# Optimization experiments

Measured on AMD Instinct MI355X. Metric: run time of the kernel, lower is better.

The kernel has to match this reference:

```python
import jax, jax.numpy as jnp
import numpy as np

N, E, H = 4096, 32768, 4
NUM_GRAPHS = 8
NEG_SLOPE_ATT = 0.2   # GATConv internal leaky_relu
NEG_SLOPE_ACT = 0.01  # F.leaky_relu default


def _glorot(k, shape):
    lim = (6.0 / (shape[0] + shape[-1])) ** 0.5
    return jax.random.uniform(k, shape, jnp.float32, -lim, lim)


def setup_inputs() -> dict:
    key = jax.random.key(0)
    ks = jax.random.split(key, 24)
    d = {}
    d["x_graph"] = jax.random.normal(ks[0], (N, 256), jnp.float32)
    d["action"] = jax.random.normal(ks[1], (N, 128), jnp.float32)
    d["temp_img"] = jax.random.normal(ks[2], (N, 128), jnp.float32)
    d["edge_attr"] = jax.random.normal(ks[3], (E, 16), jnp.float32)
    d["edge_index"] = jax.random.randint(ks[4], (2, E), 0, N)
    d["batch"] = jnp.sort(jax.random.randint(ks[5], (N,), 0, NUM_GRAPHS))
    # conv1: GATConv(512 -> 512, heads=4, edge_dim=16)
    d["W1"] = _glorot(ks[6], (512, H * 512))
    d["att_src1"] = _glorot(ks[7], (H, 512))
    d["att_dst1"] = _glorot(ks[8], (H, 512))
    d["att_edge1"] = _glorot(ks[9], (H, 512))
    d["We1"] = _glorot(ks[10], (16, H * 512))
    d["b1"] = jnp.zeros((H * 512,), jnp.float32)
    # conv2: GATConv(2048 -> 2048, heads=4, edge_dim=16)
    d["W2"] = _glorot(ks[11], (2048, H * 2048))
    d["att_src2"] = _glorot(ks[12], (H, 2048))
    d["att_dst2"] = _glorot(ks[13], (H, 2048))
    d["att_edge2"] = _glorot(ks[14], (H, 2048))
    d["We2"] = _glorot(ks[15], (16, H * 2048))
    d["b2"] = jnp.zeros((H * 2048,), jnp.float32)
    # fc_output: Linear(512*heads*heads=8192 -> 256)
    d["Wout"] = _glorot(ks[16], (8192, 256))
    d["bout"] = jnp.zeros((256,), jnp.float32)
    return d


def _gat(x, src, dst, eattr, W, a_s, a_d, a_e, We, b, C):
    # PyG GATConv: shared lin for src/dst, edge features in attention, softmax per dst.
    h = (x @ W).reshape(N, H, C)             # [N,H,C]
    ea = (eattr @ We).reshape(-1, H, C)      # [Ef,H,C]
    e = (h * a_s).sum(-1)[src] + (h * a_d).sum(-1)[dst] + (ea * a_e).sum(-1)  # [Ef,H]
    e = jax.nn.leaky_relu(e, NEG_SLOPE_ATT)
    m = jax.ops.segment_max(e, dst, num_segments=N)      # self-loops ensure every dst occupied
    ex = jnp.exp(e - m[dst])
    s = jax.ops.segment_sum(ex, dst, num_segments=N)
    alpha = ex / s[dst]                                   # [Ef,H]
    out = jax.ops.segment_sum(alpha[:, :, None] * h[src], dst, num_segments=N)  # [N,H,C]
    return out.reshape(N, H * C) + b


def _forward(x_graph, action, temp_img, edge_attr,
             W1, att_src1, att_dst1, att_edge1, We1, b1,
             W2, att_src2, att_dst2, att_edge2, We2, b2,
             Wout, bout, edge_index, batch):
    x = jnp.concatenate([x_graph, action, temp_img], axis=1)  # [N,512]
    src, dst = edge_index[0], edge_index[1]
    # add self-loops with fill_value='mean' for edge_attr (mean of incoming edge attrs)
    deg = jax.ops.segment_sum(jnp.ones((E,), x.dtype), dst, num_segments=N)
    loop_attr = jax.ops.segment_sum(edge_attr, dst, num_segments=N) / jnp.maximum(deg, 1.0)[:, None]
    loop = jnp.arange(N)
    src_f = jnp.concatenate([src, loop])
    dst_f = jnp.concatenate([dst, loop])
    ea_f = jnp.concatenate([edge_attr, loop_attr], axis=0)
    x = jax.nn.leaky_relu(_gat(x, src_f, dst_f, ea_f, W1, att_src1, att_dst1, att_edge1, We1, b1, 512), NEG_SLOPE_ACT)
    x = jax.nn.leaky_relu(_gat(x, src_f, dst_f, ea_f, W2, att_src2, att_dst2, att_edge2, We2, b2, 2048), NEG_SLOPE_ACT)
    x = jax.nn.leaky_relu(x @ Wout + bout, NEG_SLOPE_ACT)     # [N,256]
    sums = jax.ops.segment_sum(x, batch, num_segments=NUM_GRAPHS)
    cnt = jax.ops.segment_sum(jnp.ones((N,), x.dtype), batch, num_segments=NUM_GRAPHS)
    return sums / jnp.maximum(cnt, 1.0)[:, None]              # [NUM_GRAPHS,256]


def reference(x_graph, action, temp_img, edge_attr,
              W1, att_src1, att_dst1, att_edge1, We1, b1,
              W2, att_src2, att_dst2, att_edge2, We2, b2,
              Wout, bout, edge_index, batch):
    return _forward(x_graph, action, temp_img, edge_attr,
                    W1, att_src1, att_dst1, att_edge1, We1, b1,
                    W2, att_src2, att_dst2, att_edge2, We2, b2,
                    Wout, bout, edge_index, batch)
```

## Files before the change

### kernel.cpp

```cpp
#include <hip/hip_runtime.h>
#include <math.h>

constexpr int Nn  = 4096;
constexpr int Ne  = 32768;
constexpr int NEf = Ne + Nn;

constexpr size_t OFF_X    = 0;
constexpr size_t OFF_WT1H = 0;
constexpr size_t OFF_WT1L = 524288;
constexpr size_t OFF_Z1HI = 2097152;
constexpr size_t OFF_Z1LO = 6291456;
constexpr size_t OFF_X3   = 2097152;
constexpr size_t OFF_PART = 2097152;
constexpr size_t OFF_X2HI = 10485760;
constexpr size_t OFF_X2LO = 14680064;
constexpr size_t OFF_H    = 18874368;
constexpr size_t OFF_WOH  = 25165824;
constexpr size_t OFF_WOL  = 26214400;
constexpr size_t OFF_YP   = 27262976;
constexpr size_t OFF_LP  = 31457280;
constexpr size_t OFF_WS1 = OFF_LP  + 65536;
constexpr size_t OFF_WD1 = OFF_WS1 + 2048;
constexpr size_t OFF_WS2 = OFF_WD1 + 2048;
constexpr size_t OFF_WD2 = OFF_WS2 + 8192;
constexpr size_t OFF_AE1 = OFF_WD2 + 8192;
constexpr size_t OFF_AE2 = OFF_AE1 + 64;
constexpr size_t OFF_AS1 = OFF_AE2 + 64;
constexpr size_t OFF_AD1 = OFF_AS1 + 16384;
constexpr size_t OFF_AS2 = OFF_AD1 + 16384;
constexpr size_t OFF_AD2 = OFF_AS2 + 16384;
constexpr size_t OFF_EB  = OFF_AD2 + 16384;
constexpr size_t OFF_AL  = OFF_EB  + (size_t)NEf*4;
constexpr size_t OFF_I   = OFF_AL  + (size_t)NEf*4;
constexpr size_t I_DEG = 0;
constexpr size_t I_RP  = 4096;
constexpr size_t I_CUR = 8200;
constexpr size_t I_EID = 12296;
constexpr size_t WS_FLOATS = OFF_I + I_EID + (size_t)NEf + 64;

using bf16x8 = __bf16 __attribute__((ext_vector_type(8)));
using f16x8  = _Float16 __attribute__((ext_vector_type(8)));
using f32x4  = float __attribute__((ext_vector_type(4)));

__device__ __forceinline__ float wred64(float v){
#pragma unroll
  for (int o = 32; o > 0; o >>= 1) v += __shfl_down(v, o, 64);
  return v;
}
__device__ __forceinline__ float lrelu(float v, float s){ return v > 0.f ? v : s * v; }

__device__ __forceinline__ unsigned short f2bf(float x){
  unsigned int u = __float_as_uint(x);
  unsigned int r = (u + 0x7FFFu + ((u >> 16) & 1u)) >> 16;
  return (unsigned short)r;
}
__device__ __forceinline__ float bf2f(unsigned short h){
  return __uint_as_float((unsigned int)h << 16);
}
__device__ __forceinline__ void split2(float x, unsigned short& h, unsigned short& l){
  h = f2bf(x);
  l = f2bf(x - bf2f(h));
}
__device__ __forceinline__ unsigned short f2h(float x){
  _Float16 h = (_Float16)x;
  return __builtin_bit_cast(unsigned short, h);
}
__device__ __forceinline__ float h2f(unsigned short u){
  return (float)__builtin_bit_cast(_Float16, u);
}
__device__ __forceinline__ void split2h(float x, unsigned short& h, unsigned short& l){
  _Float16 hh = (_Float16)x;
  h = __builtin_bit_cast(unsigned short, hh);
  _Float16 ll = (_Float16)(x - (float)hh);
  l = __builtin_bit_cast(unsigned short, ll);
}
__device__ __forceinline__ void gload16(const void* g, void* l){
  __builtin_amdgcn_global_load_lds((const __attribute__((address_space(1))) void*)g,
                                   (__attribute__((address_space(3))) void*)l, 16, 0, 0);
}

__global__ void k_concat(const float* __restrict__ xg, const float* __restrict__ ac,
                         const float* __restrict__ ti, float* __restrict__ x){
  int i = blockIdx.x * 256 + threadIdx.x;
  int n = i >> 9, c = i & 511;
  float v;
  if (c < 256)      v = xg[(size_t)n*256 + c];
  else if (c < 384) v = ac[(size_t)n*128 + (c-256)];
  else              v = ti[(size_t)n*128 + (c-384)];
  x[i] = v;
}

__global__ void k_count(const int* __restrict__ ei, int* __restrict__ deg){
  int e = blockIdx.x * 256 + threadIdx.x;
  if (e < Ne) atomicAdd(&deg[ei[Ne + e]], 1);
}

__global__ void k_scan(const int* __restrict__ deg, int* __restrict__ rowptr, int* __restrict__ cursor){
  __shared__ int sd[1024];
  int t = threadIdx.x;
  int v[4]; int s = 0;
#pragma unroll
  for (int i = 0; i < 4; i++){ v[i] = s; s += deg[t*4 + i] + 1; }
  sd[t] = s;
  __syncthreads();
  for (int off = 1; off < 1024; off <<= 1){
    int x = (t >= off) ? sd[t - off] : 0;
    __syncthreads();
    sd[t] += x;
    __syncthreads();
  }
  int base = (t == 0) ? 0 : sd[t - 1];
#pragma unroll
  for (int i = 0; i < 4; i++){ int rp = base + v[i]; rowptr[t*4 + i] = rp; cursor[t*4 + i] = rp; }
  if (t == 1023) rowptr[4096] = sd[1023];
}

__global__ void k_fill(const int* __restrict__ ei, int* __restrict__ cursor, int* __restrict__ eids){
  int e = blockIdx.x * 256 + threadIdx.x;
  if (e >= NEf) return;
  int d = (e < Ne) ? ei[Ne + e] : (e - Ne);
  int p = atomicAdd(&cursor[d], 1);
  eids[p] = e;
}

__global__ void k_sort(const int* __restrict__ rowptr, int* __restrict__ eids){
  int n = blockIdx.x * 64 + threadIdx.x;
  if (n >= Nn) return;
  int b = rowptr[n], e = rowptr[n + 1];
  for (int i = b + 1; i < e; i++){
    int key = eids[i]; int j = i - 1;
    while (j >= b && eids[j] > key){ eids[j+1] = eids[j]; j--; }
    eids[j+1] = key;
  }
}

__global__ void k_loopattr(const float* __restrict__ eattr, const int* __restrict__ rowptr,
                           const int* __restrict__ eids, float* __restrict__ lp){
  int idx = blockIdx.x * 256 + threadIdx.x;
  int n = idx >> 4, a = idx & 15;
  if (n >= Nn) return;
  int b = rowptr[n], e = rowptr[n + 1];
  float s = 0.f; int cnt = 0;
  for (int j = b; j < e; ++j){
    int id = eids[j];
    if (id < Ne){ s += eattr[(size_t)id*16 + a]; cnt++; }
  }
  lp[(size_t)n*16 + a] = s / fmaxf((float)cnt, 1.f);
}

__global__ void k_proj(const float* __restrict__ W, const float* __restrict__ a_s,
                       const float* __restrict__ a_d, float* __restrict__ Ws,
                       float* __restrict__ Wd, int K, int C){
  int gid = blockIdx.x * 256 + threadIdx.x;
  int wave = gid >> 6, lane = gid & 63;
  int h = wave & 3, k = wave >> 2;
  if (k >= K) return;
  const float* wrow = W + (size_t)k * (4*C) + (size_t)h * C;
  const float* ar = a_s + (size_t)h * C;
  const float* dr = a_d + (size_t)h * C;
  float ps = 0.f, pd = 0.f;
  for (int c = lane; c < C; c += 64){ float w = wrow[c]; ps += w * ar[c]; pd += w * dr[c]; }
  ps = wred64(ps); pd = wred64(pd);
  if (lane == 0){ Ws[k*4 + h] = ps; Wd[k*4 + h] = pd; }
}

__global__ void k_aeproj(const float* __restrict__ We, const float* __restrict__ ae,
                         float* __restrict__ outp, int C){
  int gid = blockIdx.x * 256 + threadIdx.x;
  int wave = gid >> 6, lane = gid & 63;
  int h = wave & 3, k = wave >> 2;
  if (k >= 16) return;
  const float* wrow = We + (size_t)k * (4*C) + (size_t)h * C;
  const float* ar = ae + (size_t)h * C;
  float s = 0.f;
  for (int c = lane; c < C; c += 64) s += wrow[c] * ar[c];
  s = wred64(s);
  if (lane == 0) outp[k*4 + h] = s;
}

template<bool HALF>
__global__ __launch_bounds__(256) void k_asad(const void* __restrict__ xp, const void* __restrict__ xlp,
                      const float* __restrict__ Ws,
                      const float* __restrict__ Wd, float* __restrict__ as_,
                      float* __restrict__ ad_, int D){
  int n = blockIdx.x, t = threadIdx.x;
  float p[8] = {0,0,0,0,0,0,0,0};
  if (HALF){
    const unsigned short* rh = (const unsigned short*)xp + (size_t)n * D;
    const unsigned short* rl = (const unsigned short*)xlp + (size_t)n * D;
    for (int c = t; c < D; c += 256){
      float xv = h2f(rh[c]) + h2f(rl[c]);
      float4 ws4 = *(const float4*)&Ws[c*4];
      float4 wd4 = *(const float4*)&Wd[c*4];
      p[0] += xv * ws4.x; p[1] += xv * ws4.y; p[2] += xv * ws4.z; p[3] += xv * ws4.w;
      p[4] += xv * wd4.x; p[5] += xv * wd4.y; p[6] += xv * wd4.z; p[7] += xv * wd4.w;
    }
  } else {
    const float* row = (const float*)xp + (size_t)n * D;
    for (int c = t; c < D; c += 256){
      float xv = row[c];
      float4 ws4 = *(const float4*)&Ws[c*4];
      float4 wd4 = *(const float4*)&Wd[c*4];
      p[0] += xv * ws4.x; p[1] += xv * ws4.y; p[2] += xv * ws4.z; p[3] += xv * ws4.w;
      p[4] += xv * wd4.x; p[5] += xv * wd4.y; p[6] += xv * wd4.z; p[7] += xv * wd4.w;
    }
  }
  __shared__ float sm[4][8];
  int lane = t & 63, wid = t >> 6;
#pragma unroll
  for (int q = 0; q < 8; q++){
    float v = wred64(p[q]);
    if (lane == 0) sm[wid][q] = v;
  }
  __syncthreads();
  if (t < 8){
    float s = sm[0][t] + sm[1][t] + sm[2][t] + sm[3][t];
    if (t < 4) as_[(size_t)n*4 + t] = s;
    else       ad_[(size_t)n*4 + (t-4)] = s;
  }
}

__global__ void k_edge(const float* __restrict__ eattr, const float* __restrict__ lp,
                       const int* __restrict__ ei, const float* __restrict__ as_,
                       const float* __restrict__ ad_, const float* __restrict__ aep,
                       float* __restrict__ ebuf){
  int e = blockIdx.x * 256 + threadIdx.x;
  if (e >= NEf) return;
  int s, d; const float* ea;
  if (e < Ne){ s = ei[e]; d = ei[Ne + e]; ea = eattr + (size_t)e * 16; }
  else { s = e - Ne; d = e - Ne; ea = lp + (size_t)(e - Ne) * 16; }
  float eav[16];
#pragma unroll
  for (int k = 0; k < 16; k++) eav[k] = ea[k];
#pragma unroll
  for (int h = 0; h < 4; h++){
    float v = as_[(size_t)s*4 + h] + ad_[(size_t)d*4 + h];
#pragma unroll
    for (int k = 0; k < 16; k++) v += eav[k] * aep[k*4 + h];
    ebuf[(size_t)e*4 + h] = lrelu(v, 0.2f);
  }
}

__global__ __launch_bounds__(256) void k_softmax(const int* __restrict__ rowptr, const int* __restrict__ eids,
                          const float* __restrict__ ebuf, float* __restrict__ alpha){
  const int wid = threadIdx.x >> 6, lane = threadIdx.x & 63;
  const int n = blockIdx.x * 4 + wid;
  const int b = rowptr[n], e = rowptr[n + 1];
  float4 m = {-1e30f, -1e30f, -1e30f, -1e30f};
  for (int j = b + lane; j < e; j += 64){
    float4 ev = *(const float4*)&ebuf[(size_t)eids[j]*4];
    m.x = fmaxf(m.x, ev.x); m.y = fmaxf(m.y, ev.y);
    m.z = fmaxf(m.z, ev.z); m.w = fmaxf(m.w, ev.w);
  }
#pragma unroll
  for (int o = 32; o > 0; o >>= 1){
    m.x = fmaxf(m.x, __shfl_xor(m.x, o, 64));
    m.y = fmaxf(m.y, __shfl_xor(m.y, o, 64));
    m.z = fmaxf(m.z, __shfl_xor(m.z, o, 64));
    m.w = fmaxf(m.w, __shfl_xor(m.w, o, 64));
  }
  float4 s = {0.f, 0.f, 0.f, 0.f};
  for (int j = b + lane; j < e; j += 64){
    int eid = eids[j];
    float4 ev = *(const float4*)&ebuf[(size_t)eid*4];
    float4 ex = { expf(ev.x - m.x), expf(ev.y - m.y), expf(ev.z - m.z), expf(ev.w - m.w) };
    *(float4*)&alpha[(size_t)eid*4] = ex;
    s.x += ex.x; s.y += ex.y; s.z += ex.z; s.w += ex.w;
  }
#pragma unroll
  for (int o = 32; o > 0; o >>= 1){
    s.x += __shfl_xor(s.x, o, 64);
    s.y += __shfl_xor(s.y, o, 64);
    s.z += __shfl_xor(s.z, o, 64);
    s.w += __shfl_xor(s.w, o, 64);
  }
  float4 r = { 1.f/s.x, 1.f/s.y, 1.f/s.z, 1.f/s.w };
  for (int j = b + lane; j < e; j += 64){
    int eid = eids[j];
    float4 av = *(const float4*)&alpha[(size_t)eid*4];
    av.x *= r.x; av.y *= r.y; av.z *= r.z; av.w *= r.w;
    *(float4*)&alpha[(size_t)eid*4] = av;
  }
}

__global__ __launch_bounds__(256) void k_agg1_split(const float* __restrict__ x, const float* __restrict__ alpha,
                      const int* __restrict__ rowptr, const int* __restrict__ eids,
                      const int* __restrict__ ei, unsigned short* __restrict__ z1hi,
                      unsigned short* __restrict__ z1lo){
  int n = blockIdx.x, t = threadIdx.x;
  float2 a0 = {0,0}, a1 = {0,0}, a2 = {0,0}, a3 = {0,0};
  int b = rowptr[n], e = rowptr[n + 1];
  for (int j = b; j < e; ++j){
    int eid = eids[j];
    int s = (eid < Ne) ? ei[eid] : (eid - Ne);
    float4 av = *(const float4*)&alpha[(size_t)eid*4];
    float2 xv = *(const float2*)&x[(size_t)s*512 + t*2];
    a0.x += av.x*xv.x; a0.y += av.x*xv.y;
    a1.x += av.y*xv.x; a1.y += av.y*xv.y;
    a2.x += av.z*xv.x; a2.y += av.z*xv.y;
    a3.x += av.w*xv.x; a3.y += av.w*xv.y;
  }
  size_t base = (size_t)n*2048 + t*2;
  float2 av[4] = {a0, a1, a2, a3};
#pragma unroll
  for (int h = 0; h < 4; h++){
    ushort2 hh, ll;
    split2(av[h].x, hh.x, ll.x);
    split2(av[h].y, hh.y, ll.y);
    *(ushort2*)&z1hi[base + h*512] = hh;
    *(ushort2*)&z1lo[base + h*512] = ll;
  }
}

__global__ __launch_bounds__(256) void k_agg2b(const unsigned short* __restrict__ H,
                      const float* __restrict__ alpha,
                      const int* __restrict__ rowptr, const int* __restrict__ eids,
                      const int* __restrict__ ei, unsigned short* __restrict__ x3,
                      const float* __restrict__ b2, int h){
  int n = blockIdx.x, t = threadIdx.x;
  float acc[8] = {0,0,0,0,0,0,0,0};
  int b = rowptr[n], e = rowptr[n + 1];
  for (int j = b; j < e; ++j){
    int eid = eids[j];
    int s = (eid < Ne) ? ei[eid] : (eid - Ne);
    float a = alpha[(size_t)eid*4 + h];
    f16x8 hv = *(const f16x8*)&H[(size_t)s*2048 + t*8];
#pragma unroll
    for (int q = 0; q < 8; q++) acc[q] += a * (float)hv[q];
  }
  const float* bb = b2 + (size_t)h*2048 + t*8;
  ushort4 o0, o1;
  float4 b0 = *(const float4*)bb;
  float4 b1 = *(const float4*)(bb + 4);
  o0.x = f2h(lrelu(acc[0] + b0.x, 0.01f)); o0.y = f2h(lrelu(acc[1] + b0.y, 0.01f));
  o0.z = f2h(lrelu(acc[2] + b0.z, 0.01f)); o0.w = f2h(lrelu(acc[3] + b0.w, 0.01f));
  o1.x = f2h(lrelu(acc[4] + b1.x, 0.01f)); o1.y = f2h(lrelu(acc[5] + b1.y, 0.01f));
  o1.z = f2h(lrelu(acc[6] + b1.z, 0.01f)); o1.w = f2h(lrelu(acc[7] + b1.w, 0.01f));
  size_t base = (size_t)n*2048 + t*8;
  *(ushort4*)&x3[base]     = o0;
  *(ushort4*)&x3[base + 4] = o1;
}

template<bool HALF, bool STORELO>
__global__ __launch_bounds__(256) void k_wsplit(const float* __restrict__ W, int ldw, int coloff, int K,
                       unsigned short* __restrict__ whi, unsigned short* __restrict__ wlo){
  __shared__ float tile[32][33];
  int bk = blockIdx.x * 32, bn = blockIdx.y * 32;
  int tx = threadIdx.x & 31, ty = threadIdx.x >> 5;
#pragma unroll
  for (int i = 0; i < 4; i++){
    int k = bk + ty + i*8;
    tile[ty + i*8][tx] = W[(size_t)k*ldw + coloff + bn + tx];
  }
  __syncthreads();
#pragma unroll
  for (int i = 0; i < 4; i++){
    int n = bn + ty + i*8;
    float v = tile[tx][ty + i*8];
    unsigned short hh, ll;
    if (HALF) split2h(v, hh, ll); else split2(v, hh, ll);
    whi[(size_t)n*K + bk + tx] = hh;
    if (STORELO) wlo[(size_t)n*K + bk + tx] = ll;
  }
}

__global__ __launch_bounds__(512) void k_gemm256(
    const unsigned short* __restrict__ Ah, const unsigned short* __restrict__ Al,
    const unsigned short* __restrict__ Bh, unsigned short* __restrict__ Cout)
{
  __shared__ __align__(16) unsigned short lds[49152];
  const int t = threadIdx.x;
  const int bid = blockIdx.y * 8 + blockIdx.x;
  const int sbid = (bid & 7) * 32 + (bid >> 3);
  const int brow = (sbid >> 3) * 128, bcol = (sbid & 7) * 256;
  const int w = t >> 6, lane = t & 63;
  const int wm = (w >> 2) * 64, wn = (w & 3) * 64;
  constexpr int BUF = 16384, BOFF = 8192;

  const int asr = t >> 3;
  const int ascc = (t & 7) ^ (asr & 7);
  const unsigned short* asrc = (ascc < 4 ? Ah : Al) + (size_t)(brow + asr)*2048 + (size_t)(ascc & 3)*8;
  const int bsr = t >> 2;
  const int bscc = (t & 3) ^ ((bsr >> 1) & 3);
  const unsigned short* bsrc = Bh + (size_t)(bcol + bsr)*2048 + (size_t)bscc*8;
  const int adst = w * 512;
  const int bdst = BOFF + w * 512;

  const int fr = lane & 15, kc = lane >> 4;
  const int aswz = (kc ^ (lane & 7)) * 8;
  const int bswz = (kc ^ ((lane >> 1) & 3)) * 8;
  int aoff[4], boff[4];
#pragma unroll
  for (int m = 0; m < 4; m++) aoff[m] = (wm + m*16 + fr)*64 + aswz;
#pragma unroll
  for (int n = 0; n < 4; n++) boff[n] = BOFF + (wn + n*16 + fr)*32 + bswz;

  f32x4 acc[4][4];
#pragma unroll
  for (int m = 0; m < 4; m++)
#pragma unroll
    for (int n = 0; n < 4; n++) acc[m][n] = f32x4{0.f, 0.f, 0.f, 0.f};

  gload16(asrc,                        &lds[adst]);
  gload16(asrc + (size_t)64*2048,      &lds[4096 + adst]);
  gload16(bsrc,                        &lds[bdst]);
  gload16(bsrc + (size_t)128*2048,     &lds[4096 + bdst]);
  gload16(asrc + 32,                   &lds[BUF + adst]);
  gload16(asrc + (size_t)64*2048 + 32, &lds[BUF + 4096 + adst]);
  gload16(bsrc + 32,                   &lds[BUF + bdst]);
  gload16(bsrc + (size_t)128*2048 + 32,&lds[BUF + 4096 + bdst]);
  asm volatile("s_waitcnt vmcnt(4)" ::: "memory");
  __builtin_amdgcn_s_barrier();
  __builtin_amdgcn_sched_barrier(0);

  for (int kt = 0; kt < 64; ++kt){
    const int bufo = (kt % 3) * BUF;
    const int nbo  = ((kt + 2) % 3) * BUF;
    const size_t nko = (size_t)(kt + 2) * 32;
    const bool pf = (kt + 2) < 64;

    if (pf){
      gload16(asrc + nko,                    &lds[nbo + adst]);
      gload16(asrc + (size_t)64*2048 + nko,  &lds[nbo + 4096 + adst]);
      gload16(bsrc + nko,                    &lds[nbo + bdst]);
      gload16(bsrc + (size_t)128*2048 + nko, &lds[nbo + 4096 + bdst]);
    }

    f16x8 ah[4], al[4], bfr[4];
#pragma unroll
    for (int m = 0; m < 4; m++){
      ah[m] = *(const f16x8*)&lds[bufo + aoff[m]];
      al[m] = *(const f16x8*)&lds[bufo + (aoff[m] ^ 32)];
    }
#pragma unroll
    for (int n = 0; n < 4; n++) bfr[n] = *(const f16x8*)&lds[bufo + boff[n]];

    __builtin_amdgcn_s_setprio(1);
#pragma unroll
    for (int n = 0; n < 4; n++){
#pragma unroll
      for (int m = 0; m < 4; m++) acc[m][n] = __builtin_amdgcn_mfma_f32_16x16x32_f16(ah[m], bfr[n], acc[m][n], 0, 0, 0);
#pragma unroll
      for (int m = 0; m < 4; m++) acc[m][n] = __builtin_amdgcn_mfma_f32_16x16x32_f16(al[m], bfr[n], acc[m][n], 0, 0, 0);
    }
    __builtin_amdgcn_s_setprio(0);

    if (pf) asm volatile("s_waitcnt vmcnt(4)" ::: "memory");
    else    asm volatile("s_waitcnt vmcnt(0)" ::: "memory");
    __builtin_amdgcn_s_barrier();
    __builtin_amdgcn_sched_barrier(0);
  }

#pragma unroll
  for (int m = 0; m < 4; m++){
    const int row0 = brow + wm + m*16 + kc*4;
#pragma unroll
    for (int n = 0; n < 4; n++){
      const int col = bcol + wn + n*16 + fr;
#pragma unroll
      for (int r = 0; r < 4; r++)
        Cout[(size_t)(row0 + r)*2048 + col] = f2h(acc[m][n][r]);
    }
  }
}

template<int KLEN, bool EXACTA, bool HALF, int OUTMODE, bool BETA1, bool ACT, bool HASBIAS>
__global__ __launch_bounds__(256) void k_gemm2(
    const unsigned short* __restrict__ Ah, const unsigned short* __restrict__ Al, int lda, size_t az,
    const unsigned short* __restrict__ Bh, const unsigned short* __restrict__ Bl, int ldb, size_t bz,
    void* __restrict__ Cout, void* __restrict__ Cout2, int ldc, size_t cz,
    const float* __restrict__ bias, size_t biasz)
{
  __shared__ unsigned short lds[16384];
  const int t = threadIdx.x;
  const int z = blockIdx.z;
  const int brow = blockIdx.y * 128, bcol = blockIdx.x * 128;
  const int wid = t >> 6, lane = t & 63;
  const int wm = (wid >> 1) * 64, wn = (wid & 1) * 64;

  const int sr = t >> 3, sc = t & 7;
  const int scc = sc ^ (sr & 7);
  const unsigned short* asrc = (scc < 4 ? Ah : Al) + (size_t)(brow + sr)*lda + (size_t)z*az + (size_t)(scc & 3)*8;
  const unsigned short* bsrc = (scc < 4 ? Bh : Bl) + (size_t)(bcol + sr)*ldb + (size_t)z*bz + (size_t)(scc & 3)*8;
  unsigned short* adst = &lds[(size_t)wid * 512];
  unsigned short* bdst = &lds[8192 + (size_t)wid * 512];

  const int fr = lane & 15, kc = lane >> 4;
  const int swz = ((kc ^ (lane & 7)) << 3);
  int aoff[4], boff[4];
#pragma unroll
  for (int m = 0; m < 4; m++) aoff[m] = (wm + m*16 + fr)*64 + swz;
#pragma unroll
  for (int n = 0; n < 4; n++) boff[n] = 8192 + (wn + n*16 + fr)*64 + swz;

  f32x4 acc[4][4];
#pragma unroll
  for (int m = 0; m < 4; m++)
#pragma unroll
    for (int n = 0; n < 4; n++) acc[m][n] = f32x4{0.f, 0.f, 0.f, 0.f};

  for (int kt = 0; kt < KLEN/32; ++kt){
    const size_t ko = (size_t)kt * 32;
#pragma unroll
    for (int i = 0; i < 4; i++){
      gload16(asrc + (size_t)i*32*lda + ko, adst + i*2048);
      gload16(bsrc + (size_t)i*32*ldb + ko, bdst + i*2048);
    }
    __syncthreads();

    if (HALF){
      f16x8 ah[4], bh[4], bl[4];
#pragma unroll
      for (int m = 0; m < 4; m++) ah[m] = *(const f16x8*)&lds[aoff[m]];
#pragma unroll
      for (int n = 0; n < 4; n++){
        bh[n] = *(const f16x8*)&lds[boff[n]];
        bl[n] = *(const f16x8*)&lds[boff[n] ^ 32];
      }
#pragma unroll
      for (int m = 0; m < 4; m++)
#pragma unroll
        for (int n = 0; n < 4; n++){
          acc[m][n] = __builtin_amdgcn_mfma_f32_16x16x32_f16(ah[m], bh[n], acc[m][n], 0, 0, 0);
          acc[m][n] = __builtin_amdgcn_mfma_f32_16x16x32_f16(ah[m], bl[n], acc[m][n], 0, 0, 0);
        }
    } else {
      bf16x8 ah[4], al[4], bh[4], bl[4];
#pragma unroll
      for (int m = 0; m < 4; m++){
        ah[m] = *(const bf16x8*)&lds[aoff[m]];
        if (!EXACTA) al[m] = *(const bf16x8*)&lds[aoff[m] ^ 32];
      }
#pragma unroll
      for (int n = 0; n < 4; n++){
        bh[n] = *(const bf16x8*)&lds[boff[n]];
        bl[n] = *(const bf16x8*)&lds[boff[n] ^ 32];
      }
#pragma unroll
      for (int m = 0; m < 4; m++)
#pragma unroll
        for (int n = 0; n < 4; n++){
          acc[m][n] = __builtin_amdgcn_mfma_f32_16x16x32_bf16(ah[m], bh[n], acc[m][n], 0, 0, 0);
          acc[m][n] = __builtin_amdgcn_mfma_f32_16x16x32_bf16(ah[m], bl[n], acc[m][n], 0, 0, 0);
          if (!EXACTA)
            acc[m][n] = __builtin_amdgcn_mfma_f32_16x16x32_bf16(al[m], bh[n], acc[m][n], 0, 0, 0);
        }
    }
    __syncthreads();
  }

  float bv[4] = {0.f, 0.f, 0.f, 0.f};
  if (HASBIAS){
#pragma unroll
    for (int n = 0; n < 4; n++) bv[n] = bias[(size_t)z*biasz + bcol + wn + n*16 + fr];
  }
  float* Cf = (float*)Cout + (size_t)z*cz;
  unsigned short* Cb = (unsigned short*)Cout + (size_t)z*cz;
  unsigned short* Cl = (unsigned short*)Cout2 + (size_t)z*cz;
#pragma unroll
  for (int m = 0; m < 4; m++){
    const int row0 = brow + wm + m*16 + kc*4;
#pragma unroll
    for (int n = 0; n < 4; n++){
      const int col = bcol + wn + n*16 + fr;
#pragma unroll
      for (int r = 0; r < 4; r++){
        float v = acc[m][n][r] + bv[n];
        if (ACT) v = lrelu(v, 0.01f);
        size_t idx = (size_t)(row0 + r)*ldc + col;
        if (OUTMODE == 0){
          float* cp = &Cf[idx];
          if (BETA1) v += *cp;
          *cp = v;
        } else if (OUTMODE == 1){
          Cb[idx] = f2bf(v);
        } else {
          unsigned short hh, ll; split2h(v, hh, ll);
          Cb[idx] = hh; Cl[idx] = ll;
        }
      }
    }
  }
}

__global__ void k_gsum(const float* __restrict__ yp, const float* __restrict__ bout,
                       const int* __restrict__ batch, float* __restrict__ part){
  const int s = blockIdx.x, g = blockIdx.y, t = threadIdx.x;
  __shared__ int sb[2];
  if (t < 2){
    int key = g + t, lo = 0, hi = Nn;
    while (lo < hi){ int mid = (lo + hi) >> 1; if (batch[mid] < key) lo = mid + 1; else hi = mid; }
    sb[t] = lo;
  }
  __syncthreads();
  const int b = sb[0], e = sb[1];
  const size_t P = (size_t)Nn * 256;
  float acc = 0.f;
  float bt = bout[t];
  for (int n = b + s; n < e; n += 32){
    size_t i = (size_t)n*256 + t;
    float v = yp[i] + yp[P + i] + yp[2*P + i] + yp[3*P + i] + bt;
    acc += lrelu(v, 0.01f);
  }
  part[(size_t)(g*32 + s)*256 + t] = acc;
}

__global__ void k_gfin(const float* __restrict__ part, const int* __restrict__ batch,
                       float* __restrict__ out){
  const int g = blockIdx.x, t = threadIdx.x;
  __shared__ int sb[2];
  if (t < 2){
    int key = g + t, lo = 0, hi = Nn;
    while (lo < hi){ int mid = (lo + hi) >> 1; if (batch[mid] < key) lo = mid + 1; else hi = mid; }
    sb[t] = lo;
  }
  __syncthreads();
  const int cnt = sb[1] - sb[0];
  float s = 0.f;
#pragma unroll
  for (int k = 0; k < 32; k++) s += part[(size_t)(g*32 + k)*256 + t];
  out[g*256 + t] = s / fmaxf((float)cnt, 1.f);
}

extern "C" void kernel_launch(void* const* d_in, const int* in_sizes, int n_in,
                              void* d_out, int out_size, void* d_ws, size_t ws_size,
                              hipStream_t stream){
  const float* xg    = (const float*)d_in[0];
  const float* ac    = (const float*)d_in[1];
  const float* ti    = (const float*)d_in[2];
  const float* eattr = (const float*)d_in[3];
  const int*   ei    = (const int*)  d_in[4];
  const int*   batch = (const int*)  d_in[5];
  const float* W1    = (const float*)d_in[6];
  const float* as1w  = (const float*)d_in[7];
  const float* ad1w  = (const float*)d_in[8];
  const float* ae1w  = (const float*)d_in[9];
  const float* We1   = (const float*)d_in[10];
  const float* b1    = (const float*)d_in[11];
  const float* W2    = (const float*)d_in[12];
  const float* as2w  = (const float*)d_in[13];
  const float* ad2w  = (const float*)d_in[14];
  const float* ae2w  = (const float*)d_in[15];
  const float* We2   = (const float*)d_in[16];
  const float* b2    = (const float*)d_in[17];
  const float* Wout  = (const float*)d_in[18];
  const float* bout  = (const float*)d_in[19];
  float* out = (float*)d_out;
  float* ws  = (float*)d_ws;
  if (ws_size < WS_FLOATS * sizeof(float)) return;
  int* iws = (int*)(ws + OFF_I);

  unsigned short* z1hi = (unsigned short*)(ws + OFF_Z1HI);
  unsigned short* z1lo = (unsigned short*)(ws + OFF_Z1LO);
  unsigned short* wt1h = (unsigned short*)(ws + OFF_WT1H);
  unsigned short* wt1l = (unsigned short*)(ws + OFF_WT1L);
  unsigned short* x2hi = (unsigned short*)(ws + OFF_X2HI);
  unsigned short* x2lo = (unsigned short*)(ws + OFF_X2LO);
  unsigned short* whi  = (unsigned short*)(ws + OFF_X);
  unsigned short* woh  = (unsigned short*)(ws + OFF_WOH);
  unsigned short* wol  = (unsigned short*)(ws + OFF_WOL);
  unsigned short* Hb   = (unsigned short*)(ws + OFF_H);
  unsigned short* x3   = (unsigned short*)(ws + OFF_X3);

  hipMemsetAsync(iws + I_DEG, 0, Nn * sizeof(int), stream);
  k_concat <<<8192, 256, 0, stream>>>(xg, ac, ti, ws + OFF_X);
  k_count  <<<128,  256, 0, stream>>>(ei, iws + I_DEG);
  k_scan   <<<1,   1024, 0, stream>>>(iws + I_DEG, iws + I_RP, iws + I_CUR);
  k_fill   <<<144,  256, 0, stream>>>(ei, iws + I_CUR, iws + I_EID);
  k_sort   <<<64,    64, 0, stream>>>(iws + I_RP, iws + I_EID);
  k_loopattr<<<256, 256, 0, stream>>>(eattr, iws + I_RP, iws + I_EID, ws + OFF_LP);

  k_proj   <<<512,  256, 0, stream>>>(W1, as1w, ad1w, ws + OFF_WS1, ws + OFF_WD1, 512, 512);
  k_proj   <<<2048, 256, 0, stream>>>(W2, as2w, ad2w, ws + OFF_WS2, ws + OFF_WD2, 2048, 2048);
  k_aeproj <<<16,   256, 0, stream>>>(We1, ae1w, ws + OFF_AE1, 512);
  k_aeproj <<<16,   256, 0, stream>>>(We2, ae2w, ws + OFF_AE2, 2048);
  k_wsplit<true, true><<<dim3(256, 8), 256, 0, stream>>>(Wout, 256, 0, 8192, woh, wol);

  k_asad<false><<<4096, 256, 0, stream>>>(ws + OFF_X, nullptr, ws + OFF_WS1, ws + OFF_WD1, ws + OFF_AS1, ws + OFF_AD1, 512);
  k_edge      <<<144,  256, 0, stream>>>(eattr, ws + OFF_LP, ei, ws + OFF_AS1, ws + OFF_AD1, ws + OFF_AE1, ws + OFF_EB);
  k_softmax   <<<1024, 256, 0, stream>>>(iws + I_RP, iws + I_EID, ws + OFF_EB, ws + OFF_AL);
  k_agg1_split<<<4096, 256, 0, stream>>>(ws + OFF_X, ws + OFF_AL, iws + I_RP, iws + I_EID, ei, z1hi, z1lo);
  k_wsplit<false, true><<<dim3(16, 64), 256, 0, stream>>>(W1, 2048, 0, 512, wt1h, wt1l);
  k_gemm2<512, false, false, 2, false, true, true><<<dim3(4, 32, 4), 256, 0, stream>>>(
      z1hi, z1lo, 2048, 512,  wt1h, wt1l, 512, 512*512,
      x2hi, x2lo, 2048, 512,  b1, 512);

  k_asad<true><<<4096, 256, 0, stream>>>(x2hi, x2lo, ws + OFF_WS2, ws + OFF_WD2, ws + OFF_AS2, ws + OFF_AD2, 2048);
  k_edge   <<<144,  256, 0, stream>>>(eattr, ws + OFF_LP, ei, ws + OFF_AS2, ws + OFF_AD2, ws + OFF_AE2, ws + OFF_EB);
  k_softmax<<<1024, 256, 0, stream>>>(iws + I_RP, iws + I_EID, ws + OFF_EB, ws + OFF_AL);

  for (int h = 0; h < 4; ++h){
    k_wsplit<true, false><<<dim3(64, 64), 256, 0, stream>>>(W2, 8192, h*2048, 2048, whi, nullptr);
    k_gemm256 <<<dim3(8, 32), 512, 0, stream>>>(x2hi, x2lo, whi, Hb);
    k_agg2b   <<<4096, 256, 0, stream>>>(Hb, ws + OFF_AL, iws + I_RP, iws + I_EID, ei, x3, b2, h);
    if (h == 0)
      k_gemm2<512, true, true, 0, false, false, false><<<dim3(2, 32, 4), 256, 0, stream>>>(
          x3, x3, 2048, 512,  woh + (size_t)h*2048, wol + (size_t)h*2048, 8192, 512,
          ws + OFF_YP, nullptr, 256, (size_t)Nn*256,  nullptr, 0);
    else
      k_gemm2<512, true, true, 0, true, false, false><<<dim3(2, 32, 4), 256, 0, stream>>>(
          x3, x3, 2048, 512,  woh + (size_t)h*2048, wol + (size_t)h*2048, 8192, 512,
          ws + OFF_YP, nullptr, 256, (size_t)Nn*256,  nullptr, 0);
  }

  k_gsum<<<dim3(32, 8), 256, 0, stream>>>(ws + OFF_YP, bout, batch, ws + OFF_PART);
  k_gfin<<<8, 256, 0, stream>>>(ws + OFF_PART, batch, out);
}
```

Before: 715.9 us.

## Stage edge metadata in LDS for aggregation and double-buffer GEMM fragment registers

The two aggregation kernels now load edge ids, source indices and alpha values cooperatively into shared memory in chunks of 128. This removes the serial per-thread dependent loads (eids, then ei, then alpha) that every thread repeated for each edge. The fp16 split GEMM kernel now prefetches three K tiles ahead and double-buffers the LDS-to-register fragment loads, so the fragments for the next step are read while the MFMAs for the current step run. The cost is more registers for the second set of fragments, plus extra block barriers in the aggregation loops.

Result: faster. 695.6 us (-2.8%).

```diff
diff --git a/kernel.cpp b/kernel.cpp
--- a/kernel.cpp
+++ b/kernel.cpp
@@ -287,18 +287,28 @@
                       const int* __restrict__ rowptr, const int* __restrict__ eids,
                       const int* __restrict__ ei, unsigned short* __restrict__ z1hi,
                       unsigned short* __restrict__ z1lo){
+  __shared__ float4 sal[128];
+  __shared__ int    ssrc[128];
   int n = blockIdx.x, t = threadIdx.x;
   float2 a0 = {0,0}, a1 = {0,0}, a2 = {0,0}, a3 = {0,0};
   int b = rowptr[n], e = rowptr[n + 1];
-  for (int j = b; j < e; ++j){
-    int eid = eids[j];
-    int s = (eid < Ne) ? ei[eid] : (eid - Ne);
-    float4 av = *(const float4*)&alpha[(size_t)eid*4];
-    float2 xv = *(const float2*)&x[(size_t)s*512 + t*2];
-    a0.x += av.x*xv.x; a0.y += av.x*xv.y;
-    a1.x += av.y*xv.x; a1.y += av.y*xv.y;
-    a2.x += av.z*xv.x; a2.y += av.z*xv.y;
-    a3.x += av.w*xv.x; a3.y += av.w*xv.y;
+  for (int c0 = b; c0 < e; c0 += 128){
+    int cnt = min(e - c0, 128);
+    __syncthreads();
+    if (t < cnt){
+      int eid = eids[c0 + t];
+      ssrc[t] = (eid < Ne) ? ei[eid] : (eid - Ne);
+      sal[t]  = *(const float4*)&alpha[(size_t)eid*4];
+    }
+    __syncthreads();
+    for (int j = 0; j < cnt; ++j){
+      float4 av = sal[j];
+      float2 xv = *(const float2*)&x[(size_t)ssrc[j]*512 + t*2];
+      a0.x += av.x*xv.x; a0.y += av.x*xv.y;
+      a1.x += av.y*xv.x; a1.y += av.y*xv.y;
+      a2.x += av.z*xv.x; a2.y += av.z*xv.y;
+      a3.x += av.w*xv.x; a3.y += av.w*xv.y;
+    }
   }
   size_t base = (size_t)n*2048 + t*2;
   float2 av[4] = {a0, a1, a2, a3};
@@ -317,16 +327,26 @@
                       const int* __restrict__ rowptr, const int* __restrict__ eids,
                       const int* __restrict__ ei, unsigned short* __restrict__ x3,
                       const float* __restrict__ b2, int h){
+  __shared__ float sal[128];
+  __shared__ int   ssrc[128];
   int n = blockIdx.x, t = threadIdx.x;
   float acc[8] = {0,0,0,0,0,0,0,0};
   int b = rowptr[n], e = rowptr[n + 1];
-  for (int j = b; j < e; ++j){
-    int eid = eids[j];
-    int s = (eid < Ne) ? ei[eid] : (eid - Ne);
-    float a = alpha[(size_t)eid*4 + h];
-    f16x8 hv = *(const f16x8*)&H[(size_t)s*2048 + t*8];
-#pragma unroll
-    for (int q = 0; q < 8; q++) acc[q] += a * (float)hv[q];
+  for (int c0 = b; c0 < e; c0 += 128){
+    int cnt = min(e - c0, 128);
+    __syncthreads();
+    if (t < cnt){
+      int eid = eids[c0 + t];
+      ssrc[t] = (eid < Ne) ? ei[eid] : (eid - Ne);
+      sal[t]  = alpha[(size_t)eid*4 + h];
+    }
+    __syncthreads();
+    for (int j = 0; j < cnt; ++j){
+      float a = sal[j];
+      f16x8 hv = *(const f16x8*)&H[(size_t)ssrc[j]*2048 + t*8];
+#pragma unroll
+      for (int q = 0; q < 8; q++) acc[q] += a * (float)hv[q];
+    }
   }
   const float* bb = b2 + (size_t)h*2048 + t*8;
   ushort4 o0, o1;
@@ -401,54 +421,69 @@
 #pragma unroll
     for (int n = 0; n < 4; n++) acc[m][n] = f32x4{0.f, 0.f, 0.f, 0.f};
 
-  gload16(asrc,                        &lds[adst]);
-  gload16(asrc + (size_t)64*2048,      &lds[4096 + adst]);
-  gload16(bsrc,                        &lds[bdst]);
-  gload16(bsrc + (size_t)128*2048,     &lds[4096 + bdst]);
-  gload16(asrc + 32,                   &lds[BUF + adst]);
-  gload16(asrc + (size_t)64*2048 + 32, &lds[BUF + 4096 + adst]);
-  gload16(bsrc + 32,                   &lds[BUF + bdst]);
-  gload16(bsrc + (size_t)128*2048 + 32,&lds[BUF + 4096 + bdst]);
+  f16x8 ahA[4], alA[4], bfA[4], ahB[4], alB[4], bfB[4];
+
+#pragma unroll
+  for (int tl = 0; tl < 3; ++tl){
+    const int bb = tl * BUF;
+    const size_t ko = (size_t)tl * 32;
+    gload16(asrc + ko,                    &lds[bb + adst]);
+    gload16(asrc + (size_t)64*2048 + ko,  &lds[bb + 4096 + adst]);
+    gload16(bsrc + ko,                    &lds[bb + bdst]);
+    gload16(bsrc + (size_t)128*2048 + ko, &lds[bb + 4096 + bdst]);
+  }
   asm volatile("s_waitcnt vmcnt(4)" ::: "memory");
   __builtin_amdgcn_s_barrier();
   __builtin_amdgcn_sched_barrier(0);
-
-  for (int kt = 0; kt < 64; ++kt){
-    const int bufo = (kt % 3) * BUF;
-    const int nbo  = ((kt + 2) % 3) * BUF;
-    const size_t nko = (size_t)(kt + 2) * 32;
-    const bool pf = (kt + 2) < 64;
-
-    if (pf){
+#pragma unroll
+  for (int m = 0; m < 4; m++){
+    ahA[m] = *(const f16x8*)&lds[aoff[m]];
+    alA[m] = *(const f16x8*)&lds[aoff[m] ^ 32];
+  }
+#pragma unroll
+  for (int n = 0; n < 4; n++) bfA[n] = *(const f16x8*)&lds[boff[n]];
+  asm volatile("s_waitcnt lgkmcnt(0)" ::: "memory");
+  __builtin_amdgcn_sched_barrier(0);
+
+  auto step = [&](int kt_, f16x8 (&ahC)[4], f16x8 (&alC)[4], f16x8 (&bfC)[4],
+                          f16x8 (&ahN)[4], f16x8 (&alN)[4], f16x8 (&bfN)[4]){
+    if (kt_ + 3 < 64){
+      const int nbo = ((kt_ + 3) % 3) * BUF;
+      const size_t nko = (size_t)(kt_ + 3) * 32;
       gload16(asrc + nko,                    &lds[nbo + adst]);
       gload16(asrc + (size_t)64*2048 + nko,  &lds[nbo + 4096 + adst]);
       gload16(bsrc + nko,                    &lds[nbo + bdst]);
       gload16(bsrc + (size_t)128*2048 + nko, &lds[nbo + 4096 + bdst]);
     }
-
-    f16x8 ah[4], al[4], bfr[4];
-#pragma unroll
-    for (int m = 0; m < 4; m++){
-      ah[m] = *(const f16x8*)&lds[bufo + aoff[m]];
-      al[m] = *(const f16x8*)&lds[bufo + (aoff[m] ^ 32)];
-    }
-#pragma unroll
-    for (int n = 0; n < 4; n++) bfr[n] = *(const f16x8*)&lds[bufo + boff[n]];
-
+    if (kt_ + 1 < 64){
+      const int nxb = ((kt_ + 1) % 3) * BUF;
+#pragma unroll
+      for (int m = 0; m < 4; m++){
+        ahN[m] = *(const f16x8*)&lds[nxb + aoff[m]];
+        alN[m] = *(const f16x8*)&lds[nxb + (aoff[m] ^ 32)];
+      }
+#pragma unroll
+      for (int n = 0; n < 4; n++) bfN[n] = *(const f16x8*)&lds[nxb + boff[n]];
+    }
     __builtin_amdgcn_s_setprio(1);
 #pragma unroll
     for (int n = 0; n < 4; n++){
 #pragma unroll
-      for (int m = 0; m < 4; m++) acc[m][n] = __builtin_amdgcn_mfma_f32_16x16x32_f16(ah[m], bfr[n], acc[m][n], 0, 0, 0);
-#pragma unroll
-      for (int m = 0; m < 4; m++) acc[m][n] = __builtin_amdgcn_mfma_f32_16x16x32_f16(al[m], bfr[n], acc[m][n], 0, 0, 0);
+      for (int m = 0; m < 4; m++) acc[m][n] = __builtin_amdgcn_mfma_f32_16x16x32_f16(ahC[m], bfC[n], acc[m][n], 0, 0, 0);
+#pragma unroll
+      for (int m = 0; m < 4; m++) acc[m][n] = __builtin_amdgcn_mfma_f32_16x16x32_f16(alC[m], bfC[n], acc[m][n], 0, 0, 0);
     }
     __builtin_amdgcn_s_setprio(0);
-
-    if (pf) asm volatile("s_waitcnt vmcnt(4)" ::: "memory");
-    else    asm volatile("s_waitcnt vmcnt(0)" ::: "memory");
+    asm volatile("s_waitcnt lgkmcnt(0)" ::: "memory");
+    if (kt_ + 3 < 64) asm volatile("s_waitcnt vmcnt(4)" ::: "memory");
+    else              asm volatile("s_waitcnt vmcnt(0)" ::: "memory");
     __builtin_amdgcn_s_barrier();
     __builtin_amdgcn_sched_barrier(0);
+  };
+
+  for (int kt = 0; kt < 64; kt += 2){
+    step(kt,     ahA, alA, bfA, ahB, alB, bfB);
+    step(kt + 1, ahB, alB, bfB, ahA, alA, bfA);
   }
 
 #pragma unroll
```
